# Kernel tuning notes

Measured on AMD Instinct MI355X. Metric: run time of the kernel, lower is better.

Reference implementation:

```python
import jax, jax.numpy as jnp
import numpy as np

GRID_RES = 256          # dense stand-in for 120000-block sparse grid, grid_dim=8
CELL = 0.015            # voxel_size
ORIGIN = -0.5 * GRID_RES * CELL
S = 64                  # max_samples_per_ray
MIN_BETA = 0.015        # SDFToDensity(min_beta=voxel_size)


def _trilinear(grid, x):
    """grid: [R,R,R,5], x: [M,3] world coords -> (feat [M,5], mask [M])"""
    u = (x - ORIGIN) / CELL
    R = GRID_RES
    mask = jnp.all((u >= 0.0) & (u <= R - 1.0), axis=-1)
    i0 = jnp.clip(jnp.floor(u).astype(jnp.int32), 0, R - 2)
    f = u - i0.astype(u.dtype)                     # differentiable frac
    fx, fy, fz = f[:, 0:1], f[:, 1:2], f[:, 2:3]
    ix, iy, iz = i0[:, 0], i0[:, 1], i0[:, 2]

    def g(dx, dy, dz):
        return grid[ix + dx, iy + dy, iz + dz]      # [M,5] gather

    c00 = g(0, 0, 0) * (1 - fx) + g(1, 0, 0) * fx
    c10 = g(0, 1, 0) * (1 - fx) + g(1, 1, 0) * fx
    c01 = g(0, 0, 1) * (1 - fx) + g(1, 0, 1) * fx
    c11 = g(0, 1, 1) * (1 - fx) + g(1, 1, 1) * fx
    c0 = c00 * (1 - fy) + c10 * fy
    c1 = c01 * (1 - fy) + c11 * fy
    feat = c0 * (1 - fz) + c1 * fz
    return feat, mask


def setup_inputs() -> dict:
    key = jax.random.key(0)
    k1, k2, k3 = jax.random.split(key, 3)
    N = 4096
    grid = 0.1 * jax.random.normal(k1, (GRID_RES, GRID_RES, GRID_RES, 5), jnp.float32)
    rays_o = 0.5 * jax.random.normal(k2, (N, 3), jnp.float32)
    d = jax.random.normal(k3, (N, 3), jnp.float32)
    rays_d = d / jnp.linalg.norm(d, axis=-1, keepdims=True)
    return {
        "grid_embeddings": grid,
        "beta": jnp.array([0.03], jnp.float32),   # init_beta = 2*voxel_size
        "rays_o": rays_o,
        "rays_d": rays_d,
        "rays_d_norm": jnp.ones((N, 1), jnp.float32),
        "near": jnp.array([0.1], jnp.float32),
        "far": jnp.array([2.0], jnp.float32),
    }


def reference(grid_embeddings, beta, rays_o, rays_d, rays_d_norm, near, far):
    N = rays_o.shape[0]
    dt = (far[0] - near[0]) / S
    i = jnp.arange(S, dtype=rays_o.dtype)
    t_n = near[0] + i * dt                          # [S]
    t_f = t_n + dt
    t_mid = 0.5 * (t_n + t_f)                       # [S]

    x = rays_o[:, None, :] + t_mid[None, :, None] * rays_d[:, None, :]  # [N,S,3]
    xf = x.reshape(-1, 3)

    feat, mask = _trilinear(grid_embeddings, xf)
    sdf = feat[:, 0]                                # [N*S]
    rgb = feat[:, 1:4].reshape(N, S, 3)

    # autograd SDF gradient wrt sample positions (points independent -> grad of sum)
    sdf_grads = jax.grad(lambda xx: _trilinear(grid_embeddings, xx)[0][:, 0].sum())(xf)
    nrm = jnp.linalg.norm(sdf_grads, axis=-1, keepdims=True)
    normals = (sdf_grads / jnp.maximum(nrm, 1e-12)).reshape(N, S, 3)

    # SDFToDensity
    beta_eff = MIN_BETA + jnp.abs(beta[0])
    sigma = (1.0 / beta_eff) * (0.5 + 0.5 * jnp.sign(sdf) * jnp.expm1(-jnp.abs(sdf) / beta_eff))
    sigma = (sigma * mask.astype(sigma.dtype)).reshape(N, S)

    # nerfacc render_weight_from_density: exclusive transmittance * alpha
    tau = sigma * dt                                # [N,S]
    T = jnp.exp(-(jnp.cumsum(tau, axis=1) - tau))   # exclusive cumsum
    alpha = -jnp.expm1(-tau)
    w = T * alpha                                   # [N,S]

    rendered_rgb = jnp.einsum('ns,nsc->nc', w, rgb)
    rendered_depth = (w * t_mid[None, :]).sum(axis=1, keepdims=True) / rays_d_norm
    rendered_normals = jnp.einsum('ns,nsc->nc', w, normals)
    acc = w.sum(axis=1, keepdims=True)
    near_out = jnp.full((N, 1), near[0], rays_o.dtype) / rays_d_norm
    far_out = jnp.full((N, 1), far[0], rays_o.dtype) / rays_d_norm
    return rendered_rgb, rendered_depth, rendered_normals, acc, sdf_grads, near_out, far_out
```

## Files before the change

kernel.cpp:

```cpp
#include <hip/hip_runtime.h>


constexpr int   GRID_R   = 256;
constexpr float CELL     = 0.015f;
constexpr float ORIGIN   = -1.92f;
constexpr int   S        = 64;
constexpr float MIN_BETA = 0.015f;

__global__ __launch_bounds__(256)
void render_rays(const float* __restrict__ grid,
                 const float* __restrict__ beta_p,
                 const float* __restrict__ rays_o,
                 const float* __restrict__ rays_d,
                 const float* __restrict__ rdn,
                 const float* __restrict__ near_p,
                 const float* __restrict__ far_p,
                 float* __restrict__ out,
                 int N)
{
    const int lane = threadIdx.x & 63;
    const int ray  = blockIdx.x * (blockDim.x >> 6) + (threadIdx.x >> 6);
    if (ray >= N) return;

    const float nearv = near_p[0];
    const float farv  = far_p[0];
    const float dt    = (farv - nearv) / (float)S;
    const float t_n   = nearv + (float)lane * dt;
    const float t_mid = 0.5f * (t_n + (t_n + dt));

    const float ox = rays_o[3 * ray + 0];
    const float oy = rays_o[3 * ray + 1];
    const float oz = rays_o[3 * ray + 2];
    const float dxr = rays_d[3 * ray + 0];
    const float dyr = rays_d[3 * ray + 1];
    const float dzr = rays_d[3 * ray + 2];

    const float px = ox + t_mid * dxr;
    const float py = oy + t_mid * dyr;
    const float pz = oz + t_mid * dzr;
    const float ux = (px - ORIGIN) / CELL;
    const float uy = (py - ORIGIN) / CELL;
    const float uz = (pz - ORIGIN) / CELL;

    const bool inb = (ux >= 0.f) && (ux <= (float)(GRID_R - 1)) &&
                     (uy >= 0.f) && (uy <= (float)(GRID_R - 1)) &&
                     (uz >= 0.f) && (uz <= (float)(GRID_R - 1));

    int ix = (int)floorf(ux); ix = ix < 0 ? 0 : (ix > GRID_R - 2 ? GRID_R - 2 : ix);
    int iy = (int)floorf(uy); iy = iy < 0 ? 0 : (iy > GRID_R - 2 ? GRID_R - 2 : iy);
    int iz = (int)floorf(uz); iz = iz < 0 ? 0 : (iz > GRID_R - 2 ? GRID_R - 2 : iz);
    const float fx = ux - (float)ix;
    const float fy = uy - (float)iy;
    const float fz = uz - (float)iz;
    const float mfx = 1.f - fx, mfy = 1.f - fy, mfz = 1.f - fz;

    const float* gp = grid + (size_t)(((ix << 8) + iy) << 8 | iz) * 5;
    float v[2][2][2][4];
#pragma unroll
    for (int a = 0; a < 2; ++a)
#pragma unroll
        for (int b = 0; b < 2; ++b)
#pragma unroll
            for (int c = 0; c < 2; ++c) {
                const float* p = gp + (size_t)(((a << 8) + b) << 8 | c) * 5;
                v[a][b][c][0] = p[0];
                v[a][b][c][1] = p[1];
                v[a][b][c][2] = p[2];
                v[a][b][c][3] = p[3];
            }

    float feat[4];
    float c00_0, c10_0, c01_0, c11_0, c0_0, c1_0;
#pragma unroll
    for (int ch = 0; ch < 4; ++ch) {
        const float c00 = v[0][0][0][ch] * mfx + v[1][0][0][ch] * fx;
        const float c10 = v[0][1][0][ch] * mfx + v[1][1][0][ch] * fx;
        const float c01 = v[0][0][1][ch] * mfx + v[1][0][1][ch] * fx;
        const float c11 = v[0][1][1][ch] * mfx + v[1][1][1][ch] * fx;
        const float c0 = c00 * mfy + c10 * fy;
        const float c1 = c01 * mfy + c11 * fy;
        feat[ch] = c0 * mfz + c1 * fz;
        if (ch == 0) { c00_0 = c00; c10_0 = c10; c01_0 = c01; c11_0 = c11; c0_0 = c0; c1_0 = c1; }
    }

    const float dgx_u = ((v[1][0][0][0] - v[0][0][0][0]) * mfy + (v[1][1][0][0] - v[0][1][0][0]) * fy) * mfz +
                        ((v[1][0][1][0] - v[0][0][1][0]) * mfy + (v[1][1][1][0] - v[0][1][1][0]) * fy) * fz;
    const float dgy_u = (c10_0 - c00_0) * mfz + (c11_0 - c01_0) * fz;
    const float dgz_u = c1_0 - c0_0;
    const float gx = dgx_u / CELL;
    const float gy = dgy_u / CELL;
    const float gz = dgz_u / CELL;

    {
        float* go = out + (size_t)8 * N + ((size_t)ray * S + lane) * 3;
        go[0] = gx; go[1] = gy; go[2] = gz;
    }

    const float nrm = sqrtf(gx * gx + gy * gy + gz * gz);
    const float dn = fmaxf(nrm, 1e-12f);
    const float nx = gx / dn, ny = gy / dn, nz = gz / dn;

    const float sdf = feat[0];
    const float beta_eff = MIN_BETA + fabsf(beta_p[0]);
    const float sgn = (sdf > 0.f) ? 1.f : ((sdf < 0.f) ? -1.f : 0.f);
    float sigma = (1.f / beta_eff) * (0.5f + 0.5f * sgn * expm1f(-fabsf(sdf) / beta_eff));
    sigma = inb ? sigma : 0.f;
    const float tau = sigma * dt;

    float incl = tau;
#pragma unroll
    for (int off = 1; off < 64; off <<= 1) {
        const float t = __shfl_up(incl, off, 64);
        if (lane >= off) incl += t;
    }
    const float T     = expf(-(incl - tau));
    const float alpha = -expm1f(-tau);
    const float w     = T * alpha;

    float red[8];
    red[0] = w * feat[1];
    red[1] = w * feat[2];
    red[2] = w * feat[3];
    red[3] = w * t_mid;
    red[4] = w * nx;
    red[5] = w * ny;
    red[6] = w * nz;
    red[7] = w;
#pragma unroll
    for (int off = 32; off > 0; off >>= 1) {
#pragma unroll
        for (int k = 0; k < 8; ++k)
            red[k] += __shfl_down(red[k], off, 64);
    }

    if (lane == 0) {
        const float inv_rdn = 1.f / rdn[ray];
        out[3 * ray + 0] = red[0];
        out[3 * ray + 1] = red[1];
        out[3 * ray + 2] = red[2];
        out[(size_t)3 * N + ray] = red[3] * inv_rdn;
        out[(size_t)4 * N + 3 * ray + 0] = red[4];
        out[(size_t)4 * N + 3 * ray + 1] = red[5];
        out[(size_t)4 * N + 3 * ray + 2] = red[6];
        out[(size_t)7 * N + ray] = red[7];
        out[(size_t)200 * N + ray] = nearv * inv_rdn;
        out[(size_t)201 * N + ray] = farv * inv_rdn;
    }
}

extern "C" void kernel_launch(void* const* d_in, const int* in_sizes, int n_in,
                              void* d_out, int out_size, void* d_ws, size_t ws_size,
                              hipStream_t stream) {
    const float* grid   = (const float*)d_in[0];
    const float* beta   = (const float*)d_in[1];
    const float* rays_o = (const float*)d_in[2];
    const float* rays_d = (const float*)d_in[3];
    const float* rdn    = (const float*)d_in[4];
    const float* nearp  = (const float*)d_in[5];
    const float* farp   = (const float*)d_in[6];
    float* out = (float*)d_out;

    const int N = in_sizes[2] / 3;
    const int raysPerBlock = 4;
    const int blocks = (N + raysPerBlock - 1) / raysPerBlock;
    render_rays<<<blocks, 256, 0, stream>>>(grid, beta, rays_o, rays_d, rdn,
                                            nearp, farp, out, N);
}
```

Measured before the change: 399.7 us.

## Split trilinear corners across eight lanes per sample, one ray per block

Each ray now gets a 512-thread block in which eight lanes each gather one trilinear corner for a sample. The weighted corner values and gradient terms are summed with xor shuffles. The transmittance scan and the final reductions now span eight waves, with partial sums passed through shared memory and two barriers. The aim is more memory-level parallelism and more work in flight for the random grid gathers, in exchange for extra shuffles, block syncs and redundant per-lane math. Gradient output is written by three lanes per sample using nontemporal stores.

```diff
diff --git a/kernel.cpp b/kernel.cpp
--- a/kernel.cpp
+++ b/kernel.cpp
@@ -7,7 +7,7 @@
 constexpr int   S        = 64;
 constexpr float MIN_BETA = 0.015f;
 
-__global__ __launch_bounds__(256)
+__global__ __launch_bounds__(512, 8)
 void render_rays(const float* __restrict__ grid,
                  const float* __restrict__ beta_p,
                  const float* __restrict__ rays_o,
@@ -18,15 +18,23 @@
                  float* __restrict__ out,
                  int N)
 {
-    const int lane = threadIdx.x & 63;
-    const int ray  = blockIdx.x * (blockDim.x >> 6) + (threadIdx.x >> 6);
-    if (ray >= N) return;
+    const int ray  = blockIdx.x;
+    const int tid  = threadIdx.x;
+    const int s    = tid >> 3;
+    const int c    = tid & 7;
+    const int ca   = (c >> 2) & 1;
+    const int cb   = (c >> 1) & 1;
+    const int cc   = c & 1;
+    const int wv   = tid >> 6;
+    const int lane = tid & 63;
+
+    __shared__ float wsum[8];
+    __shared__ float redws[8][8];
 
     const float nearv = near_p[0];
     const float farv  = far_p[0];
     const float dt    = (farv - nearv) / (float)S;
-    const float t_n   = nearv + (float)lane * dt;
-    const float t_mid = 0.5f * (t_n + (t_n + dt));
+    const float t_mid = nearv + ((float)s + 0.5f) * dt;
 
     const float ox = rays_o[3 * ray + 0];
     const float oy = rays_o[3 * ray + 1];
@@ -35,12 +43,9 @@
     const float dyr = rays_d[3 * ray + 1];
     const float dzr = rays_d[3 * ray + 2];
 
-    const float px = ox + t_mid * dxr;
-    const float py = oy + t_mid * dyr;
-    const float pz = oz + t_mid * dzr;
-    const float ux = (px - ORIGIN) / CELL;
-    const float uy = (py - ORIGIN) / CELL;
-    const float uz = (pz - ORIGIN) / CELL;
+    const float ux = (ox + t_mid * dxr - ORIGIN) / CELL;
+    const float uy = (oy + t_mid * dyr - ORIGIN) / CELL;
+    const float uz = (oz + t_mid * dzr - ORIGIN) / CELL;
 
     const bool inb = (ux >= 0.f) && (ux <= (float)(GRID_R - 1)) &&
                      (uy >= 0.f) && (uy <= (float)(GRID_R - 1)) &&
@@ -52,55 +57,50 @@
     const float fx = ux - (float)ix;
     const float fy = uy - (float)iy;
     const float fz = uz - (float)iz;
-    const float mfx = 1.f - fx, mfy = 1.f - fy, mfz = 1.f - fz;
 
-    const float* gp = grid + (size_t)(((ix << 8) + iy) << 8 | iz) * 5;
-    float v[2][2][2][4];
+    const float wx = ca ? fx : 1.f - fx;   const float sx = ca ? 1.f : -1.f;
+    const float wy = cb ? fy : 1.f - fy;   const float sy = cb ? 1.f : -1.f;
+    const float wz = cc ? fz : 1.f - fz;   const float sz = cc ? 1.f : -1.f;
+
+    const int cell = (((ix + ca) << 8) + (iy + cb) << 8) + (iz + cc);
+    const float* p = grid + (size_t)cell * 5;
+    const float v0 = p[0], v1 = p[1], v2 = p[2], v3 = p[3];
+
+    const float w3 = wx * wy * wz;
+    float r0 = w3 * v0;
+    float r1 = w3 * v1;
+    float r2 = w3 * v2;
+    float r3 = w3 * v3;
+    float g0 = sx * wy * wz * v0;
+    float g1 = wx * sy * wz * v0;
+    float g2 = wx * wy * sz * v0;
+
 #pragma unroll
-    for (int a = 0; a < 2; ++a)
-#pragma unroll
-        for (int b = 0; b < 2; ++b)
-#pragma unroll
-            for (int c = 0; c < 2; ++c) {
-                const float* p = gp + (size_t)(((a << 8) + b) << 8 | c) * 5;
-                v[a][b][c][0] = p[0];
-                v[a][b][c][1] = p[1];
-                v[a][b][c][2] = p[2];
-                v[a][b][c][3] = p[3];
-            }
-
-    float feat[4];
-    float c00_0, c10_0, c01_0, c11_0, c0_0, c1_0;
-#pragma unroll
-    for (int ch = 0; ch < 4; ++ch) {
-        const float c00 = v[0][0][0][ch] * mfx + v[1][0][0][ch] * fx;
-        const float c10 = v[0][1][0][ch] * mfx + v[1][1][0][ch] * fx;
-        const float c01 = v[0][0][1][ch] * mfx + v[1][0][1][ch] * fx;
-        const float c11 = v[0][1][1][ch] * mfx + v[1][1][1][ch] * fx;
-        const float c0 = c00 * mfy + c10 * fy;
-        const float c1 = c01 * mfy + c11 * fy;
-        feat[ch] = c0 * mfz + c1 * fz;
-        if (ch == 0) { c00_0 = c00; c10_0 = c10; c01_0 = c01; c11_0 = c11; c0_0 = c0; c1_0 = c1; }
+    for (int off = 1; off < 8; off <<= 1) {
+        r0 += __shfl_xor(r0, off, 64);
+        r1 += __shfl_xor(r1, off, 64);
+        r2 += __shfl_xor(r2, off, 64);
+        r3 += __shfl_xor(r3, off, 64);
+        g0 += __shfl_xor(g0, off, 64);
+        g1 += __shfl_xor(g1, off, 64);
+        g2 += __shfl_xor(g2, off, 64);
     }
 
-    const float dgx_u = ((v[1][0][0][0] - v[0][0][0][0]) * mfy + (v[1][1][0][0] - v[0][1][0][0]) * fy) * mfz +
-                        ((v[1][0][1][0] - v[0][0][1][0]) * mfy + (v[1][1][1][0] - v[0][1][1][0]) * fy) * fz;
-    const float dgy_u = (c10_0 - c00_0) * mfz + (c11_0 - c01_0) * fz;
-    const float dgz_u = c1_0 - c0_0;
-    const float gx = dgx_u / CELL;
-    const float gy = dgy_u / CELL;
-    const float gz = dgz_u / CELL;
+    const float gx = g0 / CELL;
+    const float gy = g1 / CELL;
+    const float gz = g2 / CELL;
 
-    {
-        float* go = out + (size_t)8 * N + ((size_t)ray * S + lane) * 3;
-        go[0] = gx; go[1] = gy; go[2] = gz;
+    if (c < 3) {
+        const float gval = (c == 0) ? gx : ((c == 1) ? gy : gz);
+        __builtin_nontemporal_store(gval,
+            out + (size_t)8 * N + ((size_t)ray * S + s) * 3 + c);
     }
 
     const float nrm = sqrtf(gx * gx + gy * gy + gz * gz);
-    const float dn = fmaxf(nrm, 1e-12f);
+    const float dn  = fmaxf(nrm, 1e-12f);
     const float nx = gx / dn, ny = gy / dn, nz = gz / dn;
 
-    const float sdf = feat[0];
+    const float sdf = r0;
     const float beta_eff = MIN_BETA + fabsf(beta_p[0]);
     const float sgn = (sdf > 0.f) ? 1.f : ((sdf < 0.f) ? -1.f : 0.f);
     float sigma = (1.f / beta_eff) * (0.5f + 0.5f * sgn * expm1f(-fabsf(sdf) / beta_eff));
@@ -109,42 +109,57 @@
 
     float incl = tau;
 #pragma unroll
-    for (int off = 1; off < 64; off <<= 1) {
+    for (int off = 8; off < 64; off <<= 1) {
         const float t = __shfl_up(incl, off, 64);
         if (lane >= off) incl += t;
     }
-    const float T     = expf(-(incl - tau));
+    if (lane == 63) wsum[wv] = incl;
+    __syncthreads();
+    float pre = 0.f;
+#pragma unroll
+    for (int k = 0; k < 7; ++k) pre += (wv > k) ? wsum[k] : 0.f;
+    const float cum = pre + incl;
+
+    const float T     = expf(-(cum - tau));
     const float alpha = -expm1f(-tau);
-    const float w     = T * alpha;
+    const float wgt   = T * alpha;
 
     float red[8];
-    red[0] = w * feat[1];
-    red[1] = w * feat[2];
-    red[2] = w * feat[3];
-    red[3] = w * t_mid;
-    red[4] = w * nx;
-    red[5] = w * ny;
-    red[6] = w * nz;
-    red[7] = w;
+    red[0] = wgt * r1;
+    red[1] = wgt * r2;
+    red[2] = wgt * r3;
+    red[3] = wgt * t_mid;
+    red[4] = wgt * nx;
+    red[5] = wgt * ny;
+    red[6] = wgt * nz;
+    red[7] = wgt;
 #pragma unroll
-    for (int off = 32; off > 0; off >>= 1) {
+    for (int off = 8; off < 64; off <<= 1) {
 #pragma unroll
         for (int k = 0; k < 8; ++k)
-            red[k] += __shfl_down(red[k], off, 64);
+            red[k] += __shfl_xor(red[k], off, 64);
     }
+    if (lane == 0) {
+#pragma unroll
+        for (int k = 0; k < 8; ++k) redws[wv][k] = red[k];
+    }
+    __syncthreads();
 
-    if (lane == 0) {
+    if (tid < 10) {
         const float inv_rdn = 1.f / rdn[ray];
-        out[3 * ray + 0] = red[0];
-        out[3 * ray + 1] = red[1];
-        out[3 * ray + 2] = red[2];
-        out[(size_t)3 * N + ray] = red[3] * inv_rdn;
-        out[(size_t)4 * N + 3 * ray + 0] = red[4];
-        out[(size_t)4 * N + 3 * ray + 1] = red[5];
-        out[(size_t)4 * N + 3 * ray + 2] = red[6];
-        out[(size_t)7 * N + ray] = red[7];
-        out[(size_t)200 * N + ray] = nearv * inv_rdn;
-        out[(size_t)201 * N + ray] = farv * inv_rdn;
+        if (tid < 8) {
+            float v = 0.f;
+#pragma unroll
+            for (int k = 0; k < 8; ++k) v += redws[k][tid];
+            if (tid < 3)       out[3 * ray + tid] = v;
+            else if (tid == 3) out[(size_t)3 * N + ray] = v * inv_rdn;
+            else if (tid < 7)  out[(size_t)4 * N + 3 * ray + (tid - 4)] = v;
+            else               out[(size_t)7 * N + ray] = v;
+        } else if (tid == 8) {
+            out[(size_t)200 * N + ray] = nearv * inv_rdn;
+        } else {
+            out[(size_t)201 * N + ray] = farv * inv_rdn;
+        }
     }
 }
 
@@ -161,8 +176,6 @@
     float* out = (float*)d_out;
 
     const int N = in_sizes[2] / 3;
-    const int raysPerBlock = 4;
-    const int blocks = (N + raysPerBlock - 1) / raysPerBlock;
-    render_rays<<<blocks, 256, 0, stream>>>(grid, beta, rays_o, rays_d, rdn,
-                                            nearp, farp, out, N);
+    render_rays<<<N, 512, 0, stream>>>(grid, beta, rays_o, rays_d, rdn,
+                                       nearp, farp, out, N);
 }
```

New measurement: 400.5 us. About the same (+0.2%).
